# Kernel optimization log

Hardware: AMD Instinct MI355X
Metric: run time of the kernel (lower is better)

## Reference

```python
import jax, jax.numpy as jnp
import numpy as np

B, S, D, H = 4, 2048, 1024, 16
HD = D // H  # head dim = 64

def setup_inputs() -> dict:
    key = jax.random.key(0)
    k1, k2, k3 = jax.random.split(key, 3)
    x = jax.random.normal(k1, (B, S, D), dtype=jnp.float32)
    W_attn = jax.random.normal(k2, (D, 3 * D), dtype=jnp.float32) * 0.02
    b_attn = jnp.zeros((3 * D,), dtype=jnp.float32)
    W_proj = jax.random.normal(k3, (D, D), dtype=jnp.float32) * 0.02
    b_proj = jnp.zeros((D,), dtype=jnp.float32)
    return {"x": x, "W_attn": W_attn, "b_attn": b_attn, "W_proj": W_proj, "b_proj": b_proj}

def reference(x, W_attn, b_attn, W_proj, b_proj):
    b, s, d = x.shape
    qkv = x @ W_attn + b_attn                       # [b, s, 3d]
    q, k, v = jnp.split(qkv, 3, axis=-1)
    # [b, s, d] -> [b, h, s, hd]
    def heads(t):
        return t.reshape(b, s, H, HD).transpose(0, 2, 1, 3)
    q, k, v = heads(q), heads(k), heads(v)
    scale = 1.0 / jnp.sqrt(jnp.asarray(HD, dtype=x.dtype))
    scores = jnp.einsum('bhqd,bhkd->bhqk', q, k) * scale  # [b, h, s, s]
    causal = jnp.tril(jnp.ones((s, s), dtype=bool))
    scores = jnp.where(causal[None, None, :, :], scores, jnp.asarray(-jnp.inf, dtype=x.dtype))
    attn = jax.nn.softmax(scores, axis=-1)
    out = jnp.einsum('bhqk,bhkd->bhqd', attn, v)    # [b, h, s, hd]
    out = out.transpose(0, 2, 1, 3).reshape(b, s, d)
    return out @ W_proj + b_proj
```

## Files before the change

kernel.cpp:

```cpp
#include <hip/hip_runtime.h>
#include <hip/hip_bf16.h>
#include <stdint.h>

#define B_  4
#define S_  2048
#define D_  1024
#define H_  16
#define HD_ 64

typedef __attribute__((ext_vector_type(8))) short          s16x8;
typedef __attribute__((ext_vector_type(4))) float          f32x4;
typedef __attribute__((ext_vector_type(8))) unsigned short u16x8;

__device__ __forceinline__ unsigned short f2bf(float f) {
  union { float f; unsigned int u; } v; v.f = f;
  unsigned int u = v.u;
  u += 0x7fffu + ((u >> 16) & 1u);
  return (unsigned short)(u >> 16);
}

__device__ __forceinline__ float max3f(float a, float b, float c) {
  float d;
  asm("v_max3_f32 %0, %1, %2, %3" : "=v"(d) : "v"(a), "v"(b), "v"(c));
  return d;
}

#if __has_builtin(__builtin_amdgcn_exp2f)
#define EXP2(x) __builtin_amdgcn_exp2f(x)
#else
#define EXP2(x) exp2f(x)
#endif

#define GLDS16(g, l)                                                           \
  __builtin_amdgcn_global_load_lds(                                            \
      (const __attribute__((address_space(1))) void*)(g),                      \
      (__attribute__((address_space(3))) void*)(l), 16, 0, 0)

__global__ void k_cvt(const float* __restrict__ src, unsigned short* __restrict__ dst, int n4) {
  int i = blockIdx.x * blockDim.x + threadIdx.x;
  int stride = gridDim.x * blockDim.x;
  for (int j = i; j < n4; j += stride) {
    float4 v = reinterpret_cast<const float4*>(src)[j];
    ushort4 o;
    o.x = f2bf(v.x); o.y = f2bf(v.y); o.z = f2bf(v.z); o.w = f2bf(v.w);
    reinterpret_cast<ushort4*>(dst)[j] = o;
  }
}

__global__ void k_tpose_cvt(const float* __restrict__ src, unsigned short* __restrict__ dst,
                            int R, int C) {
  __shared__ unsigned short tile[64][72];
  int c0 = blockIdx.x * 64, r0 = blockIdx.y * 64;
  int tx = threadIdx.x & 63, ty = threadIdx.x >> 6;
#pragma unroll
  for (int i = 0; i < 16; ++i) {
    int r = ty * 16 + i;
    tile[r][tx] = f2bf(src[(size_t)(r0 + r) * C + c0 + tx]);
  }
  __syncthreads();
#pragma unroll
  for (int i = 0; i < 16; ++i) {
    int c = ty * 16 + i;
    dst[(size_t)(c0 + c) * R + r0 + tx] = tile[tx][c];
  }
}

__global__ void k_tpose_v(const unsigned short* __restrict__ src, unsigned short* __restrict__ dst) {
  __shared__ unsigned short tile[64][72];
  int s0 = blockIdx.x * 64, bh = blockIdx.y;
  int tx = threadIdx.x & 63, ty = threadIdx.x >> 6;
  const unsigned short* sb = src + (size_t)bh * S_ * HD_;
  unsigned short*       db = dst + (size_t)bh * S_ * HD_;
#pragma unroll
  for (int i = 0; i < 16; ++i) {
    int r = ty * 16 + i;
    tile[r][tx] = sb[(size_t)(s0 + r) * HD_ + tx];
  }
  __syncthreads();
#pragma unroll
  for (int i = 0; i < 16; ++i) {
    int hd = ty * 16 + i;
    db[(size_t)hd * S_ + s0 + tx] = tile[tx][hd];
  }
}

__device__ __forceinline__ void gemm_core(const unsigned short* __restrict__ A,
                                          const unsigned short* __restrict__ Bt,
                                          int K, int m0, int n0,
                                          unsigned short* sm, f32x4 acc[4][4]) {
  const int t = threadIdx.x;
  const int w = t >> 6, l = t & 63;
  const int wm = w >> 1, wn = w & 1;
  const int lo = l & 15, hi = l >> 4;

  const int ci0 = w * 64 + l, ci1 = ci0 + 256;
  const int rA0 = ci0 >> 2, cA0 = (ci0 & 3) ^ ((rA0 >> 1) & 3);
  const int rA1 = ci1 >> 2, cA1 = (ci1 & 3) ^ ((rA1 >> 1) & 3);
  const unsigned short* gA0 = A  + (size_t)(m0 + rA0) * K + cA0 * 8;
  const unsigned short* gA1 = A  + (size_t)(m0 + rA1) * K + cA1 * 8;
  const unsigned short* gB0 = Bt + (size_t)(n0 + rA0) * K + cA0 * 8;
  const unsigned short* gB1 = Bt + (size_t)(n0 + rA1) * K + cA1 * 8;
  const int ldsA0 = (w * 64) * 8;
  const int ldsA1 = (256 + w * 64) * 8;

#pragma unroll
  for (int m = 0; m < 4; ++m)
#pragma unroll
    for (int n = 0; n < 4; ++n)
      acc[m][n] = (f32x4){0.f, 0.f, 0.f, 0.f};

  const int NT = K >> 5;

  {
    unsigned short* b = sm;
    GLDS16(gA0, b + ldsA0);
    GLDS16(gA1, b + ldsA1);
    GLDS16(gB0, b + 4096 + ldsA0);
    GLDS16(gB1, b + 4096 + ldsA1);
  }

  for (int kt = 0; kt < NT; ++kt) {
    __syncthreads();
    if (kt + 1 < NT) {
      unsigned short* b = sm + ((kt + 1) & 1) * 8192;
      const int ko = (kt + 1) << 5;
      GLDS16(gA0 + ko, b + ldsA0);
      GLDS16(gA1 + ko, b + ldsA1);
      GLDS16(gB0 + ko, b + 4096 + ldsA0);
      GLDS16(gB1 + ko, b + 4096 + ldsA1);
    }
    const unsigned short* Ab = sm + (kt & 1) * 8192;
    const unsigned short* Bb = Ab + 4096;
    s16x8 af[4], bfr[4];
#pragma unroll
    for (int m = 0; m < 4; ++m) {
      int row = wm * 64 + m * 16 + lo;
      af[m] = *(const s16x8*)(Ab + row * 32 + ((hi ^ ((row >> 1) & 3)) << 3));
    }
#pragma unroll
    for (int n = 0; n < 4; ++n) {
      int row = wn * 64 + n * 16 + lo;
      bfr[n] = *(const s16x8*)(Bb + row * 32 + ((hi ^ ((row >> 1) & 3)) << 3));
    }
    __builtin_amdgcn_s_setprio(1);
#pragma unroll
    for (int m = 0; m < 4; ++m)
#pragma unroll
      for (int n = 0; n < 4; ++n)
        acc[m][n] = __builtin_amdgcn_mfma_f32_16x16x32_bf16(af[m], bfr[n], acc[m][n], 0, 0, 0);
    __builtin_amdgcn_s_setprio(0);
  }
}

__global__ __launch_bounds__(256, 3)
void k_gemm_qkv(const unsigned short* __restrict__ A, const unsigned short* __restrict__ Bt,
                const float* __restrict__ bias,
                unsigned short* __restrict__ Qh, unsigned short* __restrict__ Kh,
                unsigned short* __restrict__ Vh) {
  __shared__ unsigned short sm[2 * 8192];
  const int bid = blockIdx.x;
  const int i = bid >> 3;
  const int x = (bid & 7) * 3 + (i % 3);
  const int y = i / 3;
  const int m0 = y * 128, n0 = x * 128;
  f32x4 acc[4][4];
  gemm_core(A, Bt, 1024, m0, n0, sm, acc);
  const int t = threadIdx.x, w = t >> 6, l = t & 63;
  const int wm = w >> 1, wn = w & 1, lo = l & 15, hi = l >> 4;
#pragma unroll
  for (int m = 0; m < 4; ++m)
#pragma unroll
    for (int n = 0; n < 4; ++n) {
      int col = n0 + wn * 64 + n * 16 + lo;
      float bv = bias[col];
      int sel = col >> 10, cw = col & 1023, h = cw >> 6, hd = cw & 63;
      float scl = (sel == 0) ? 0.18033688011112042f : 1.0f;
      unsigned short* dst = (sel == 0) ? Qh : ((sel == 1) ? Kh : Vh);
#pragma unroll
      for (int r = 0; r < 4; ++r) {
        int row = m0 + wm * 64 + m * 16 + hi * 4 + r;
        int b = row >> 11, s = row & 2047;
        dst[(((size_t)b * H_ + h) * S_ + s) * HD_ + hd] = f2bf((acc[m][n][r] + bv) * scl);
      }
    }
}

__global__ __launch_bounds__(256, 3)
void k_gemm_proj(const unsigned short* __restrict__ A, const unsigned short* __restrict__ Bt,
                 const float* __restrict__ bias, float* __restrict__ C, int N) {
  __shared__ unsigned short sm[2 * 8192];
  const int bid = blockIdx.x;
  const int x = bid & 7, y = bid >> 3;
  const int m0 = y * 128, n0 = x * 128;
  f32x4 acc[4][4];
  gemm_core(A, Bt, 1024, m0, n0, sm, acc);
  const int t = threadIdx.x, w = t >> 6, l = t & 63;
  const int wm = w >> 1, wn = w & 1, lo = l & 15, hi = l >> 4;
#pragma unroll
  for (int m = 0; m < 4; ++m)
#pragma unroll
    for (int n = 0; n < 4; ++n) {
      int col = n0 + wn * 64 + n * 16 + lo;
      float bv = bias[col];
#pragma unroll
      for (int r = 0; r < 4; ++r) {
        int row = m0 + wm * 64 + m * 16 + hi * 4 + r;
        C[(size_t)row * N + col] = acc[m][n][r] + bv;
      }
    }
}

__global__ __launch_bounds__(256, 2)
void k_attn(const unsigned short* __restrict__ Qh, const unsigned short* __restrict__ Kh,
            const unsigned short* __restrict__ Vt, unsigned short* __restrict__ ctx) {
  __shared__ unsigned short Kl[2 * 4096];
  __shared__ unsigned short Vl[2 * 4096];
  const int bid = blockIdx.x;
  const int g8  = bid & 7;
  const int idx = bid >> 3;
  const int bh  = g8 * 8 + (idx & 7);
  const int jp  = idx >> 3;
  const int t = threadIdx.x, w = t >> 6, l = t & 63, lo = l & 15, hi = l >> 4;
  const unsigned short* Qb = Qh + (size_t)bh * S_ * HD_;
  const unsigned short* Kb = Kh + (size_t)bh * S_ * HD_;
  const unsigned short* Vb = Vt + (size_t)bh * S_ * HD_;
  const int bb = bh >> 4, h = bh & 15;

  const int r0s = t >> 3, schunk = t & 7, r1s = r0s + 32;
  const int ks0 = ((r0s & 1) << 4) | ((r0s >> 1) & 15);
  const int ks1 = 32 | ((r1s & 1) << 4) | ((r1s >> 1) & 15);
  const int kd0 = ks0 * 64 + 8 * (schunk ^ (ks0 & 7));
  const int kd1 = ks1 * 64 + 8 * (schunk ^ (ks1 & 7));
  const int vd0 = r0s * 64 + 8 * (schunk ^ (r0s & 7));
  const int vd1 = r1s * 64 + 8 * (schunk ^ (r1s & 7));
  const unsigned short* ksrc0 = Kb + r0s * HD_ + schunk * 8;
  const unsigned short* ksrc1 = Kb + r1s * HD_ + schunk * 8;
  const unsigned short* vsrc0 = Vb + (size_t)r0s * S_ + schunk * 8;
  const unsigned short* vsrc1 = Vb + (size_t)r1s * S_ + schunk * 8;

  const int e0  = jp + 1;
  const int ex1 = 32 - jp;
  const int nv  = (ex1 + 1) >> 1;

  s16x8 qf[2][2];
  int qbase[2];
  qbase[0] = 64 * jp        + w * 16;
  qbase[1] = 64 * (31 - jp) + w * 16;
#pragma unroll
  for (int g = 0; g < 2; ++g)
#pragma unroll
    for (int kk = 0; kk < 2; ++kk)
      qf[g][kk] = *(const s16x8*)(Qb + (size_t)(qbase[g] + lo) * HD_ + kk * 32 + hi * 8);

  f32x4 O[2][4];
#pragma unroll
  for (int g = 0; g < 2; ++g)
#pragma unroll
    for (int nh = 0; nh < 4; ++nh) O[g][nh] = (f32x4){0.f, 0.f, 0.f, 0.f};
  float mrun[2] = {-1e30f, -1e30f}, lrun[2] = {0.f, 0.f};
  const f32x4 fz = {0.f, 0.f, 0.f, 0.f};

  auto process = [&](int kv0, int sub, bool g0act) {
    const unsigned short* Kbuf = Kl + sub * 4096;
    const unsigned short* Vbuf = Vl + sub * 4096;
    f32x4 p[2][4];
    {
      s16x8 kf[4];
#pragma unroll
      for (int n = 0; n < 4; ++n)
        kf[n] = *(const s16x8*)&Kbuf[(n * 16 + lo) * 64 + 8 * (hi ^ (lo & 7))];
      __builtin_amdgcn_s_setprio(1);
#pragma unroll
      for (int n = 0; n < 4; ++n)
        p[1][n] = __builtin_amdgcn_mfma_f32_16x16x32_bf16(kf[n], qf[1][0], fz, 0, 0, 0);
      if (g0act) {
#pragma unroll
        for (int n = 0; n < 4; ++n)
          p[0][n] = __builtin_amdgcn_mfma_f32_16x16x32_bf16(kf[n], qf[0][0], fz, 0, 0, 0);
      }
      __builtin_amdgcn_s_setprio(0);
    }
    {
      s16x8 kf[4];
#pragma unroll
      for (int n = 0; n < 4; ++n)
        kf[n] = *(const s16x8*)&Kbuf[(n * 16 + lo) * 64 + 8 * ((4 + hi) ^ (lo & 7))];
      __builtin_amdgcn_s_setprio(1);
#pragma unroll
      for (int n = 0; n < 4; ++n)
        p[1][n] = __builtin_amdgcn_mfma_f32_16x16x32_bf16(kf[n], qf[1][1], p[1][n], 0, 0, 0);
      if (g0act) {
#pragma unroll
        for (int n = 0; n < 4; ++n)
          p[0][n] = __builtin_amdgcn_mfma_f32_16x16x32_bf16(kf[n], qf[0][1], p[0][n], 0, 0, 0);
      }
      __builtin_amdgcn_s_setprio(0);
    }

    union PU { unsigned int u[4]; s16x8 s; };
    PU pa[2][2];
#pragma unroll
    for (int g = 0; g < 2; ++g) {
      if (g == 0 && !g0act) continue;
      if (kv0 + 63 > qbase[g]) {
        const int q = qbase[g] + lo;
#pragma unroll
        for (int n = 0; n < 4; ++n)
#pragma unroll
          for (int r = 0; r < 4; ++r) {
            int kv = kv0 + 32 * (n >> 1) + 8 * hi + 2 * r + (n & 1);
            p[g][n][r] = (kv <= q) ? p[g][n][r] : -1e30f;
          }
      }
      float a0 = max3f(p[g][0][0], p[g][0][1], p[g][0][2]);
      float a1 = max3f(p[g][0][3], p[g][1][0], p[g][1][1]);
      float a2 = max3f(p[g][1][2], p[g][1][3], p[g][2][0]);
      float a3 = max3f(p[g][2][1], p[g][2][2], p[g][2][3]);
      float a4 = max3f(p[g][3][0], p[g][3][1], p[g][3][2]);
      float mx = fmaxf(max3f(a0, a1, a2), max3f(a3, a4, p[g][3][3]));
      const bool need = !__all(mx <= mrun[g] + 8.0f);
      if (need) {
        mx = fmaxf(mx, __shfl_xor(mx, 16));
        mx = fmaxf(mx, __shfl_xor(mx, 32));
        float mnew = fmaxf(mrun[g], mx);
        float alpha = EXP2(mrun[g] - mnew);
        mrun[g] = mnew;
        lrun[g] *= alpha;
#pragma unroll
        for (int r = 0; r < 4; ++r) {
          float ar_ = __shfl(alpha, 4 * hi + r);
#pragma unroll
          for (int nh = 0; nh < 4; ++nh) O[g][nh][r] *= ar_;
        }
      }
      const float mr = mrun[g];
      float s0 = 0.f, s1 = 0.f, s2 = 0.f, s3 = 0.f;
#pragma unroll
      for (int n = 0; n < 4; ++n) {
        float e0_ = EXP2(p[g][n][0] - mr);
        float e1_ = EXP2(p[g][n][1] - mr);
        float e2_ = EXP2(p[g][n][2] - mr);
        float e3_ = EXP2(p[g][n][3] - mr);
        p[g][n][0] = e0_; p[g][n][1] = e1_;
        p[g][n][2] = e2_; p[g][n][3] = e3_;
        s0 += e0_; s1 += e1_; s2 += e2_; s3 += e3_;
      }
      lrun[g] += (s0 + s1) + (s2 + s3);
#pragma unroll
      for (int c = 0; c < 2; ++c)
#pragma unroll
        for (int r = 0; r < 4; ++r) {
          unsigned int pk;
          asm("v_cvt_pk_bf16_f32 %0, %1, %2"
              : "=v"(pk) : "v"(p[g][2 * c][r]), "v"(p[g][2 * c + 1][r]));
          pa[g][c].u[r] = pk;
        }
    }

#pragma unroll
    for (int c = 0; c < 2; ++c) {
      s16x8 vf[4];
#pragma unroll
      for (int nh = 0; nh < 4; ++nh)
        vf[nh] = *(const s16x8*)&Vbuf[(nh * 16 + lo) * 64 + 8 * ((4 * c + hi) ^ (lo & 7))];
      __builtin_amdgcn_s_setprio(1);
#pragma unroll
      for (int nh = 0; nh < 4; ++nh)
        O[1][nh] = __builtin_amdgcn_mfma_f32_16x16x32_bf16(pa[1][c].s, vf[nh], O[1][nh], 0, 0, 0);
      if (g0act) {
#pragma unroll
        for (int nh = 0; nh < 4; ++nh)
          O[0][nh] = __builtin_amdgcn_mfma_f32_16x16x32_bf16(pa[0][c].s, vf[nh], O[0][nh], 0, 0, 0);
      }
      __builtin_amdgcn_s_setprio(0);
    }
  };

  u16x8 rk00 = *(const u16x8*)ksrc0;
  u16x8 rk01 = *(const u16x8*)ksrc1;
  u16x8 rk10 = *(const u16x8*)(ksrc0 + (size_t)64 * HD_);
  u16x8 rk11 = *(const u16x8*)(ksrc1 + (size_t)64 * HD_);
  u16x8 rv00 = *(const u16x8*)vsrc0;
  u16x8 rv01 = *(const u16x8*)vsrc1;
  u16x8 rv10 = *(const u16x8*)(vsrc0 + 64);
  u16x8 rv11 = *(const u16x8*)(vsrc1 + 64);
  *(u16x8*)&Kl[kd0] = rk00;        *(u16x8*)&Kl[kd1] = rk01;
  *(u16x8*)&Kl[4096 + kd0] = rk10; *(u16x8*)&Kl[4096 + kd1] = rk11;
  *(u16x8*)&Vl[vd0] = rv00;        *(u16x8*)&Vl[vd1] = rv01;
  *(u16x8*)&Vl[4096 + vd0] = rv10; *(u16x8*)&Vl[4096 + vd1] = rv11;
  __syncthreads();

  for (int kt = 0; kt < nv; ++kt) {
    const int base = kt * 128;
    const bool pf = (kt + 1 < nv);
    if (pf) {
      const int nb = base + 128;
      rk00 = *(const u16x8*)(ksrc0 + (size_t)nb * HD_);
      rk01 = *(const u16x8*)(ksrc1 + (size_t)nb * HD_);
      rk10 = *(const u16x8*)(ksrc0 + (size_t)(nb + 64) * HD_);
      rk11 = *(const u16x8*)(ksrc1 + (size_t)(nb + 64) * HD_);
      rv00 = *(const u16x8*)(vsrc0 + nb);
      rv01 = *(const u16x8*)(vsrc1 + nb);
      rv10 = *(const u16x8*)(vsrc0 + nb + 64);
      rv11 = *(const u16x8*)(vsrc1 + nb + 64);
    }

    process(base, 0, 2 * kt < e0);
    if (2 * kt + 1 < ex1)
      process(base + 64, 1, 2 * kt + 1 < e0);

    if (pf) {
      __syncthreads();
      *(u16x8*)&Kl[kd0] = rk00;        *(u16x8*)&Kl[kd1] = rk01;
      *(u16x8*)&Kl[4096 + kd0] = rk10; *(u16x8*)&Kl[4096 + kd1] = rk11;
      *(u16x8*)&Vl[vd0] = rv00;        *(u16x8*)&Vl[vd1] = rv01;
      *(u16x8*)&Vl[4096 + vd0] = rv10; *(u16x8*)&Vl[4096 + vd1] = rv11;
      __syncthreads();
    }
  }

#pragma unroll
  for (int g = 0; g < 2; ++g) {
    float lr = lrun[g];
    lr += __shfl_xor(lr, 16);
    lr += __shfl_xor(lr, 32);
#pragma unroll
    for (int r = 0; r < 4; ++r) {
      float li = 1.0f / __shfl(lr, 4 * hi + r);
      int qg = qbase[g] + 4 * hi + r;
#pragma unroll
      for (int nh = 0; nh < 4; ++nh) {
        int hd = nh * 16 + lo;
        ctx[(((size_t)(bb * S_ + qg)) * H_ + h) * HD_ + hd] = f2bf(O[g][nh][r] * li);
      }
    }
  }
}

extern "C" void kernel_launch(void* const* d_in, const int* in_sizes, int n_in,
                              void* d_out, int out_size, void* d_ws, size_t ws_size,
                              hipStream_t stream) {
  const float* x      = (const float*)d_in[0];
  const float* W_attn = (const float*)d_in[1];
  const float* b_attn = (const float*)d_in[2];
  const float* W_proj = (const float*)d_in[3];
  const float* b_proj = (const float*)d_in[4];
  float* out = (float*)d_out;

  char* ws = (char*)d_ws;
  size_t off = 0;
  auto alloc = [&](size_t bytes) {
    char* p = ws + off;
    off += (bytes + 255) & ~(size_t)255;
    return p;
  };
  unsigned short* xb  = (unsigned short*)alloc((size_t)8192 * 1024 * 2);
  unsigned short* Wta = (unsigned short*)alloc((size_t)3072 * 1024 * 2);
  unsigned short* Wtp = (unsigned short*)alloc((size_t)1024 * 1024 * 2);
  unsigned short* Qh  = (unsigned short*)alloc((size_t)64 * 2048 * 64 * 2);
  unsigned short* Kh  = (unsigned short*)alloc((size_t)64 * 2048 * 64 * 2);
  unsigned short* Vh  = (unsigned short*)alloc((size_t)64 * 2048 * 64 * 2);
  unsigned short* Vt  = (unsigned short*)alloc((size_t)64 * 2048 * 64 * 2);
  unsigned short* ctx = (unsigned short*)alloc((size_t)8192 * 1024 * 2);

  k_cvt<<<dim3(2048), dim3(256), 0, stream>>>(x, xb, (8192 * 1024) / 4);
  k_tpose_cvt<<<dim3(48, 16), dim3(256), 0, stream>>>(W_attn, Wta, 1024, 3072);
  k_tpose_cvt<<<dim3(16, 16), dim3(256), 0, stream>>>(W_proj, Wtp, 1024, 1024);
  k_gemm_qkv<<<dim3(1536), dim3(256), 0, stream>>>(xb, Wta, b_attn, Qh, Kh, Vh);
  k_tpose_v<<<dim3(32, 64), dim3(256), 0, stream>>>(Vh, Vt);
  k_attn<<<dim3(1024), dim3(256), 0, stream>>>(Qh, Kh, Vt, ctx);
  k_gemm_proj<<<dim3(512), dim3(256), 0, stream>>>(ctx, Wtp, b_proj, out, 1024);
}
```

Measured before the change: 172.4 us.

## Enlarge QKV GEMM tile to 256x128 with 512-thread blocks

The QKV projection GEMM switches from 128x128 tiles with 256 threads to 256x128 tiles with 512 threads (8 waves), halving the grid. The B tile loaded into LDS is now shared across twice as many rows, which cuts global and LDS traffic per output element. Launch bounds drop to one block per CU-slot with a larger LDS footprint, which lowers occupancy and latency hiding. The row-to-block mapping (y from bid) was kept, so the tile indexing must still cover all 8192 rows with 768 blocks.

```diff
diff --git a/kernel.cpp b/kernel.cpp
--- a/kernel.cpp
+++ b/kernel.cpp
@@ -152,21 +152,81 @@
   }
 }
 
-__global__ __launch_bounds__(256, 3)
+__global__ __launch_bounds__(512, 1)
 void k_gemm_qkv(const unsigned short* __restrict__ A, const unsigned short* __restrict__ Bt,
                 const float* __restrict__ bias,
                 unsigned short* __restrict__ Qh, unsigned short* __restrict__ Kh,
                 unsigned short* __restrict__ Vh) {
-  __shared__ unsigned short sm[2 * 8192];
+  __shared__ unsigned short sm[2 * 12288];
   const int bid = blockIdx.x;
   const int i = bid >> 3;
   const int x = (bid & 7) * 3 + (i % 3);
   const int y = i / 3;
-  const int m0 = y * 128, n0 = x * 128;
+  const int m0 = y * 256, n0 = x * 128;
+  const int K = 1024;
+
+  const int t = threadIdx.x;
+  const int w = t >> 6, l = t & 63;
+  const int wm = w >> 1, wn = w & 1;
+  const int lo = l & 15, hi = l >> 4;
+
+  const int rA0 = t >> 2,         cA0 = (t & 3) ^ ((rA0 >> 1) & 3);
+  const int ci1 = t + 512;
+  const int rA1 = ci1 >> 2,       cA1 = (ci1 & 3) ^ ((rA1 >> 1) & 3);
+  const int rB  = t >> 2,         cB  = (t & 3) ^ ((rB >> 1) & 3);
+  const unsigned short* gA0 = A  + (size_t)(m0 + rA0) * K + cA0 * 8;
+  const unsigned short* gA1 = A  + (size_t)(m0 + rA1) * K + cA1 * 8;
+  const unsigned short* gB  = Bt + (size_t)(n0 + rB)  * K + cB  * 8;
+  const int ldsA0 = (w * 64) * 8;
+  const int ldsA1 = (512 + w * 64) * 8;
+  const int ldsB  = 8192 + (w * 64) * 8;
+
   f32x4 acc[4][4];
-  gemm_core(A, Bt, 1024, m0, n0, sm, acc);
-  const int t = threadIdx.x, w = t >> 6, l = t & 63;
-  const int wm = w >> 1, wn = w & 1, lo = l & 15, hi = l >> 4;
+#pragma unroll
+  for (int m = 0; m < 4; ++m)
+#pragma unroll
+    for (int n = 0; n < 4; ++n)
+      acc[m][n] = (f32x4){0.f, 0.f, 0.f, 0.f};
+
+  const int NT = K >> 5;
+  {
+    unsigned short* b = sm;
+    GLDS16(gA0, b + ldsA0);
+    GLDS16(gA1, b + ldsA1);
+    GLDS16(gB,  b + ldsB);
+  }
+
+  for (int kt = 0; kt < NT; ++kt) {
+    __syncthreads();
+    if (kt + 1 < NT) {
+      unsigned short* b = sm + ((kt + 1) & 1) * 12288;
+      const int ko = (kt + 1) << 5;
+      GLDS16(gA0 + ko, b + ldsA0);
+      GLDS16(gA1 + ko, b + ldsA1);
+      GLDS16(gB  + ko, b + ldsB);
+    }
+    const unsigned short* Ab = sm + (kt & 1) * 12288;
+    const unsigned short* Bb = Ab + 8192;
+    s16x8 af[4], bfr[4];
+#pragma unroll
+    for (int m = 0; m < 4; ++m) {
+      int row = wm * 64 + m * 16 + lo;
+      af[m] = *(const s16x8*)(Ab + row * 32 + ((hi ^ ((row >> 1) & 3)) << 3));
+    }
+#pragma unroll
+    for (int n = 0; n < 4; ++n) {
+      int row = wn * 64 + n * 16 + lo;
+      bfr[n] = *(const s16x8*)(Bb + row * 32 + ((hi ^ ((row >> 1) & 3)) << 3));
+    }
+    __builtin_amdgcn_s_setprio(1);
+#pragma unroll
+    for (int m = 0; m < 4; ++m)
+#pragma unroll
+      for (int n = 0; n < 4; ++n)
+        acc[m][n] = __builtin_amdgcn_mfma_f32_16x16x32_bf16(af[m], bfr[n], acc[m][n], 0, 0, 0);
+    __builtin_amdgcn_s_setprio(0);
+  }
+
 #pragma unroll
   for (int m = 0; m < 4; ++m)
 #pragma unroll
@@ -466,7 +526,7 @@
   k_cvt<<<dim3(2048), dim3(256), 0, stream>>>(x, xb, (8192 * 1024) / 4);
   k_tpose_cvt<<<dim3(48, 16), dim3(256), 0, stream>>>(W_attn, Wta, 1024, 3072);
   k_tpose_cvt<<<dim3(16, 16), dim3(256), 0, stream>>>(W_proj, Wtp, 1024, 1024);
-  k_gemm_qkv<<<dim3(1536), dim3(256), 0, stream>>>(xb, Wta, b_attn, Qh, Kh, Vh);
+  k_gemm_qkv<<<dim3(768), dim3(512), 0, stream>>>(xb, Wta, b_attn, Qh, Kh, Vh);
   k_tpose_v<<<dim3(32, 64), dim3(256), 0, stream>>>(Vh, Vt);
   k_attn<<<dim3(1024), dim3(256), 0, stream>>>(Qh, Kh, Vt, ctx);
   k_gemm_proj<<<dim3(512), dim3(256), 0, stream>>>(ctx, Wtp, b_proj, out, 1024);
```

Result: no change. 169.7 us (-1.5%).
